# Kernel tuning notes

Hardware: AMD Instinct MI355X
Metric: run time of the kernel (lower is better)

The kernel has to match this reference:

```python
import jax, jax.numpy as jnp
import numpy as np

NUM_CLASSES = 10
CLS_W, L1_W, GIOU_W = 2.0, 5.0, 2.0


def box_cxcywh_to_xyxy(b):
    cx, cy, w, h = b[..., 0], b[..., 1], b[..., 2], b[..., 3]
    return jnp.stack([cx - w / 2, cy - h / 2, cx + w / 2, cy + h / 2], axis=-1)


def giou_matrix(b1, b2):
    # b1: (B,N,4), b2: (B,M,4) xyxy -> (B,N,M)
    a1 = jnp.clip(b1[..., 2] - b1[..., 0], 0) * jnp.clip(b1[..., 3] - b1[..., 1], 0)
    a2 = jnp.clip(b2[..., 2] - b2[..., 0], 0) * jnp.clip(b2[..., 3] - b2[..., 1], 0)
    lt = jnp.maximum(b1[..., :, None, :2], b2[..., None, :, :2])
    rb = jnp.minimum(b1[..., :, None, 2:], b2[..., None, :, 2:])
    wh = jnp.clip(rb - lt, 0)
    inter = wh[..., 0] * wh[..., 1]
    union = a1[..., :, None] + a2[..., None, :] - inter
    iou = inter / jnp.clip(union, 1e-6)
    lte = jnp.minimum(b1[..., :, None, :2], b2[..., None, :, :2])
    rbe = jnp.maximum(b1[..., :, None, 2:], b2[..., None, :, 2:])
    whe = jnp.clip(rbe - lte, 0)
    enc = whe[..., 0] * whe[..., 1]
    return iou - (enc - union) / jnp.clip(enc, 1e-6)


def giou_elem(b1, b2):
    # b1, b2: (N,4) xyxy, paired -> (N,)
    a1 = jnp.clip(b1[:, 2] - b1[:, 0], 0) * jnp.clip(b1[:, 3] - b1[:, 1], 0)
    a2 = jnp.clip(b2[:, 2] - b2[:, 0], 0) * jnp.clip(b2[:, 3] - b2[:, 1], 0)
    lt = jnp.maximum(b1[:, :2], b2[:, :2])
    rb = jnp.minimum(b1[:, 2:], b2[:, 2:])
    wh = jnp.clip(rb - lt, 0)
    inter = wh[:, 0] * wh[:, 1]
    union = a1 + a2 - inter
    iou = inter / jnp.clip(union, 1e-6)
    lte = jnp.minimum(b1[:, :2], b2[:, :2])
    rbe = jnp.maximum(b1[:, 2:], b2[:, 2:])
    whe = jnp.clip(rbe - lte, 0)
    enc = whe[:, 0] * whe[:, 1]
    return iou - (enc - union) / jnp.clip(enc, 1e-6)


def hungarian(cost):
    # Jonker-Volgenant style shortest-augmenting-path assignment (== scipy.linear_sum_assignment)
    cost = np.asarray(cost, dtype=np.float64)
    transposed = cost.shape[0] > cost.shape[1]
    C = cost.T if transposed else cost
    n, m = C.shape  # n <= m
    u = np.zeros(n + 1)
    v = np.zeros(m + 1)
    p = np.zeros(m + 1, dtype=np.int64)
    colr = np.arange(m + 1)
    for i in range(1, n + 1):
        p[0] = i
        j0 = 0
        minv = np.full(m + 1, np.inf)
        way = np.zeros(m + 1, dtype=np.int64)
        used = np.zeros(m + 1, dtype=bool)
        while True:
            used[j0] = True
            i0 = p[j0]
            unused = colr[1:][~used[1:]]
            cur = C[i0 - 1, unused - 1] - u[i0] - v[unused]
            better = cur < minv[unused]
            bidx = unused[better]
            minv[bidx] = cur[better]
            way[bidx] = j0
            j1 = unused[np.argmin(minv[unused])]
            delta = minv[j1]
            u[p[used]] += delta
            v[used] -= delta
            minv[~used] -= delta
            j0 = j1
            if p[j0] == 0:
                break
        while j0 != 0:
            jn = way[j0]
            p[j0] = p[jn]
            j0 = jn
    rows = p[1:] - 1
    cols = np.arange(m)
    sel = rows >= 0
    r, c = rows[sel], cols[sel]
    if transposed:
        r, c = c, r
    order = np.argsort(r)
    return r[order], c[order]


def compute_matches(pred_logits, pred_boxes, gt_classes, gt_boxes):
    # Batched cost matrices on device, per-sample Hungarian on host (mirrors torch.no_grad matcher).
    B, Q, _ = pred_logits.shape
    G = gt_classes.shape[1]
    prob = jax.nn.softmax(pred_logits, axis=-1)
    cls_idx = jnp.clip(gt_classes, 0, NUM_CLASSES - 1)
    idx = jnp.broadcast_to(cls_idx[:, None, :], (B, Q, G))
    cls_cost = -jnp.take_along_axis(prob, idx, axis=2)                 # (B,Q,G)
    l1_cost = jnp.abs(pred_boxes[:, :, None, :] - gt_boxes[:, None, :, :]).sum(-1)
    g = giou_matrix(box_cxcywh_to_xyxy(pred_boxes), box_cxcywh_to_xyxy(gt_boxes))
    cost = CLS_W * cls_cost + L1_W * l1_cost - GIOU_W * g
    cost_np = np.asarray(jax.device_get(cost))
    valid_np = np.asarray(jax.device_get(gt_classes)) >= 0
    bs, ps, gs = [], [], []
    for bi in range(B):
        vidx = np.nonzero(valid_np[bi])[0]
        if vidx.size == 0:
            continue
        r, c = hungarian(cost_np[bi][:, vidx])
        bs.append(np.full(r.size, bi, dtype=np.int64))
        ps.append(r.astype(np.int64))
        gs.append(vidx[c].astype(np.int64))
    if bs:
        return np.concatenate(bs), np.concatenate(ps), np.concatenate(gs)
    z = np.zeros(0, np.int64)
    return z, z, z


def detection_loss(pred_logits, pred_boxes, gt_boxes, target_cls, b_f, p_f, g_f, n_matched):
    C1 = pred_logits.shape[-1]
    logp = jax.nn.log_softmax(pred_logits, axis=-1).reshape(-1, C1)
    t = target_cls.reshape(-1)
    w = jnp.ones(C1, dtype=pred_logits.dtype).at[-1].set(0.1)
    nll = -jnp.take_along_axis(logp, t[:, None], axis=1)[:, 0]
    wt = w[t]
    cls_loss = (wt * nll).sum() / wt.sum()
    mp = pred_boxes[b_f, p_f]
    mg = gt_boxes[b_f, g_f]
    l1 = jnp.abs(mp - mg).sum()
    gd = giou_elem(box_cxcywh_to_xyxy(mp), box_cxcywh_to_xyxy(mg))
    gl = (1.0 - gd).sum()
    return CLS_W * cls_loss + L1_W * l1 / n_matched + GIOU_W * gl / n_matched


def setup_inputs() -> dict:
    key = jax.random.key(0)
    k1, k2, k3, k4, k5 = jax.random.split(key, 5)
    B, Q, G, C = 64, 900, 100, NUM_CLASSES
    pred_logits = jax.random.normal(k1, (B, Q, C + 1), dtype=jnp.float32)
    pred_boxes = jax.random.uniform(k2, (B, Q, 4), dtype=jnp.float32, minval=0.05, maxval=0.6)
    gt_boxes = jax.random.uniform(k3, (B, G, 4), dtype=jnp.float32, minval=0.05, maxval=0.6)
    cls = jax.random.randint(k4, (B, G), 0, C)
    nvalid = jax.random.randint(k5, (B,), 1, G + 1)
    mask = jnp.arange(G)[None, :] < nvalid[:, None]
    gt_classes = jnp.where(mask, cls, -1).astype(jnp.int32)
    return {"pred_logits": pred_logits, "pred_boxes": pred_boxes,
            "gt_classes": gt_classes, "gt_boxes": gt_boxes}


def reference(pred_logits, pred_boxes, gt_classes, gt_boxes):
    B, Q = pred_logits.shape[:2]
    b_f, p_f, g_f = compute_matches(pred_logits, pred_boxes, gt_classes, gt_boxes)
    gt_np = np.asarray(jax.device_get(gt_classes))
    tc = np.full((B, Q), NUM_CLASSES, dtype=np.int32)
    tc[b_f, p_f] = gt_np[b_f, g_f]
    n_matched = max(int(b_f.size), 1)
    return detection_loss(pred_logits, pred_boxes, gt_boxes, jnp.asarray(tc), b_f, p_f, g_f, n_matched)
```

## Files before the change

### kernel.cpp

```cpp
#include <hip/hip_runtime.h>
#include <hip/hip_bf16.h>
#include <math.h>

#define BB 64
#define QQ 900
#define GG 100
#define NCLS 10
#define CP1 11

#define STRIDE 960
#define KPL 15
#define NT 512
#define NW 8
#define QMASK 255
#define ROUND_CAP 20000

#define NCH 8
#define QCH 128

#define CLS_W 2.0f
#define L1_W 5.0f
#define GIOU_W 2.0f

struct Accum {
  double wnll, wt, l1, gl;
  int nm, counter;
  int pad[6];
};

__global__ __launch_bounds__(256) void cost_kernel(
    const float* __restrict__ logits, const float* __restrict__ pboxes,
    const int* __restrict__ gcls, const float* __restrict__ gboxes,
    float* __restrict__ cost, float4* __restrict__ part, Accum* acc) {
  const int b = blockIdx.y;
  const int chunk = blockIdx.x;
  const int tid = threadIdx.x;
  const int ql = tid & (QCH - 1);
  const int gh = tid >> 7;
  const int q = chunk * QCH + ql;

  if (chunk == 0 && b == 0 && tid == 0) {
    acc->wnll = 0.0; acc->wt = 0.0; acc->l1 = 0.0; acc->gl = 0.0;
    acc->nm = 0; acc->counter = 0;
  }

  __shared__ float s_gb[GG * 4];
  __shared__ int   s_gc[GG];
  __shared__ float s_prob[QCH * 13];
  __shared__ float s_c[GG][QCH + 1];
  __shared__ int   sh_n;

  if (tid == 0) sh_n = 0;
  __syncthreads();

  for (int i = tid; i < GG * 4; i += 256) s_gb[i] = gboxes[b * GG * 4 + i];
  for (int i = tid; i < GG; i += 256) {
    const int v = gcls[b * GG + i];
    s_gc[i] = v;
    if (v >= 0) atomicAdd(&sh_n, 1);
  }

  float pcx = 0.f, pcy = 0.f, pw = 0.f, ph = 0.f;
  if (q < QQ) {
    const float* pb = pboxes + ((size_t)b * QQ + q) * 4;
    pcx = pb[0]; pcy = pb[1]; pw = pb[2]; ph = pb[3];
    if (gh == 0) {
      const float* lg = logits + ((size_t)b * QQ + q) * CP1;
      float l[CP1];
      float mx = -1e30f;
      for (int c = 0; c < CP1; ++c) { l[c] = lg[c]; mx = fmaxf(mx, l[c]); }
      float se = 0.f;
      for (int c = 0; c < CP1; ++c) { l[c] = expf(l[c] - mx); se += l[c]; }
      const float inv = 1.0f / se;
      for (int c = 0; c < NCLS; ++c) s_prob[ql * 13 + c] = l[c] * inv;
    }
  }
  __syncthreads();
  const int sn = sh_n;

  const float px1 = pcx - 0.5f * pw, py1 = pcy - 0.5f * ph;
  const float px2 = pcx + 0.5f * pw, py2 = pcy + 0.5f * ph;
  const float pa = fmaxf(px2 - px1, 0.f) * fmaxf(py2 - py1, 0.f);

  float* crow = cost + ((size_t)b * GG) * STRIDE + q;
  for (int g = gh; g < sn; g += 2) {
    float cv = 3e38f;
    if (q < QQ) {
      int cls = s_gc[g];
      cls = cls < 0 ? 0 : (cls > NCLS - 1 ? NCLS - 1 : cls);
      const float cc = -s_prob[ql * 13 + cls];
      const float gcx = s_gb[g * 4 + 0], gcy = s_gb[g * 4 + 1];
      const float gw  = s_gb[g * 4 + 2], gh2 = s_gb[g * 4 + 3];
      const float l1 = fabsf(pcx - gcx) + fabsf(pcy - gcy) + fabsf(pw - gw) + fabsf(ph - gh2);
      const float gx1 = gcx - 0.5f * gw, gy1 = gcy - 0.5f * gh2;
      const float gx2 = gcx + 0.5f * gw, gy2 = gcy + 0.5f * gh2;
      const float ga = fmaxf(gx2 - gx1, 0.f) * fmaxf(gy2 - gy1, 0.f);
      const float ltx = fmaxf(px1, gx1), lty = fmaxf(py1, gy1);
      const float rbx = fminf(px2, gx2), rby = fminf(py2, gy2);
      const float iw = fmaxf(rbx - ltx, 0.f), ih = fmaxf(rby - lty, 0.f);
      const float inter = iw * ih;
      const float uni = pa + ga - inter;
      const float iou = inter / fmaxf(uni, 1e-6f);
      const float ex1 = fminf(px1, gx1), ey1 = fminf(py1, gy1);
      const float ex2 = fmaxf(px2, gx2), ey2 = fmaxf(py2, gy2);
      const float ew = fmaxf(ex2 - ex1, 0.f), eh = fmaxf(ey2 - ey1, 0.f);
      const float enc = ew * eh;
      const float giou = iou - (enc - uni) / fmaxf(enc, 1e-6f);
      cv = CLS_W * cc + L1_W * l1 - GIOU_W * giou;
      crow[(size_t)g * STRIDE] = cv;
    } else if (q < STRIDE) {
      crow[(size_t)g * STRIDE] = 1e30f;
    }
    s_c[g][ql] = cv;
  }
  __syncthreads();

  if (tid < sn) {
    const int kmax = (chunk == NCH - 1) ? (QQ - (NCH - 1) * QCH) : QCH;
    float m1 = 3e38f, m2 = 3e38f, n1 = 3e38f, n2 = 3e38f;
    int j1 = 0x7FFFFFFF, i1 = 0x7FFFFFFF;
    const int ka = kmax < 64 ? kmax : 64;
    for (int k = 0; k < ka; ++k) {
      const float c = s_c[tid][k];
      if (c < m1) { m2 = m1; m1 = c; j1 = 1 + chunk * QCH + k; }
      else if (c < m2) m2 = c;
    }
    for (int k = 64; k < kmax; ++k) {
      const float c = s_c[tid][k];
      if (c < n1) { n2 = n1; n1 = c; i1 = 1 + chunk * QCH + k; }
      else if (c < n2) n2 = c;
    }
    if (n1 < m1) { m2 = fminf(m1, n2); m1 = n1; j1 = i1; }
    else m2 = fminf(m2, n1);
    part[((size_t)b * NCH + chunk) * QCH + tid] = make_float4(m1, m2, __int_as_float(j1), 0.f);
  }
}

__global__ __launch_bounds__(NT) void jv_kernel(
    const float* __restrict__ logits, const float* __restrict__ pboxes,
    const int* __restrict__ gcls, const float* __restrict__ gboxes,
    const float* __restrict__ cost, const float4* __restrict__ part,
    Accum* acc, float* out) {
  const int b = blockIdx.x;
  const int tid = threadIdx.x;
  const int lane = tid & 63;
  const int w = tid >> 6;

  __shared__ float vl[STRIDE + 2];
  __shared__ int   p[QQ + 1];
  __shared__ unsigned long long way64[STRIDE + 2];
  __shared__ float m1l[GG + 1], m2l[GG + 1];
  __shared__ int   aminl[GG + 1];
  __shared__ int   s_gc[GG];
  __shared__ int   queue[QMASK + 1];
  __shared__ int   sh_n, sh_qtail, sh_head;
  __shared__ double r0[NW], r1[NW], r2[NW], r3[NW];
  __shared__ int r4[NW];
  __shared__ float s_lse[QQ], s_mx[QQ];

  if (tid == 0) { sh_n = 0; sh_qtail = 0; sh_head = 0; }
  for (int j = tid; j <= QQ; j += NT) p[j] = 0;
  for (int j = tid; j < STRIDE + 2; j += NT) { vl[j] = 0.f; way64[j] = 0ull; }
  if (tid < GG) s_gc[tid] = gcls[b * GG + tid];
  __syncthreads();
  if (tid < GG && s_gc[tid] >= 0) atomicAdd(&sh_n, 1);
  __syncthreads();
  const int n = sh_n;
  const float* Cb = cost + (size_t)b * GG * STRIDE;

  for (int r = tid; r < n; r += NT) {
    float m1 = 3e38f, m2 = 3e38f;
    int j1 = 0x7FFFFFFF;
#pragma unroll
    for (int ch = 0; ch < NCH; ++ch) {
      const float4 pr = part[((size_t)b * NCH + ch) * QCH + r];
      const float pm1 = pr.x, pm2 = pr.y;
      if (pm1 < m1) { m2 = fminf(m1, pm2); m1 = pm1; j1 = __float_as_int(pr.z); }
      else m2 = fminf(m2, pm1);
    }
    m1l[r] = m1; m2l[r] = m2; aminl[r] = j1;
  }
  for (int qq = tid; qq < QQ; qq += NT) {
    const float* lg = logits + ((size_t)b * QQ + qq) * CP1;
    float l[CP1];
    float mx = -1e30f;
    for (int c = 0; c < CP1; ++c) { l[c] = lg[c]; mx = fmaxf(mx, l[c]); }
    float se = 0.f;
    for (int c = 0; c < CP1; ++c) se += expf(l[c] - mx);
    s_mx[qq] = mx;
    s_lse[qq] = logf(se);
  }
  __syncthreads();

  if (tid < n) {
    const float regret = m2l[tid] - m1l[tid];
    const unsigned long long key =
        ((unsigned long long)__float_as_uint(regret) << 20) | (unsigned long long)(tid + 1);
    atomicMax(&way64[aminl[tid]], key);
  }
  __syncthreads();
  if (tid < n) {
    const int j1 = aminl[tid];
    if ((int)(way64[j1] & 0xFFFFFu) == tid + 1) {
      p[j1] = tid + 1;
      vl[j1] = m1l[tid] - m2l[tid];
    } else {
      const int t0 = atomicAdd(&sh_qtail, 1);
      queue[t0 & QMASK] = tid + 1;
    }
  }
  __syncthreads();

  {
    float pf[KPL];
    int pf_ok = 0, pf_rid = 0;
    int rounds = 0;
    while (rounds < ROUND_CAP) {
      const int head = sh_head, tail = sh_qtail;
      const int nq = tail - head;
      if (nq <= 0) break;
      const int take = nq < NW ? nq : NW;
      float m1 = 3e38f, m2 = 3e38f;
      int j1 = 0x7FFFFFFF, rid = 0;
      if (w < take) {
        float rc[KPL];
        if (pf_ok) {
          rid = pf_rid;
#pragma unroll
          for (int k = 0; k < KPL; ++k) rc[k] = pf[k];
        } else {
          rid = queue[(head + w) & QMASK];
          const float* Cr = Cb + (size_t)(rid - 1) * STRIDE + lane;
#pragma unroll
          for (int k = 0; k < KPL; ++k) rc[k] = Cr[k << 6];
        }
        float n1 = 3e38f, n2 = 3e38f;
        int i1 = 0x7FFFFFFF;
#pragma unroll
        for (int k = 0; k < 8; ++k) {
          const float c = rc[k] - vl[1 + lane + (k << 6)];
          if (c < m1) { m2 = m1; m1 = c; j1 = 1 + lane + (k << 6); }
          else if (c < m2) m2 = c;
        }
#pragma unroll
        for (int k = 8; k < KPL; ++k) {
          const float c = rc[k] - vl[1 + lane + (k << 6)];
          if (c < n1) { n2 = n1; n1 = c; i1 = 1 + lane + (k << 6); }
          else if (c < n2) n2 = c;
        }
        if (n1 < m1) { m2 = fminf(m1, n2); m1 = n1; j1 = i1; }
        else m2 = fminf(m2, n1);
        for (int m = 1; m < 64; m <<= 1) {
          const float o1 = __shfl_xor(m1, m);
          const float o2 = __shfl_xor(m2, m);
          const int oj = __shfl_xor(j1, m);
          if (o1 < m1) { m2 = fminf(m1, o2); m1 = o1; j1 = oj; }
          else m2 = fminf(m2, o1);
        }
      }
      pf_ok = 0;
      const int npos = head + take + w;
      if (npos < tail) {
        pf_rid = queue[npos & QMASK];
        const float* Cr = Cb + (size_t)(pf_rid - 1) * STRIDE + lane;
#pragma unroll
        for (int k = 0; k < KPL; ++k) pf[k] = Cr[k << 6];
        pf_ok = 1;
      }
      if (take > 1) {
        if (w < take && lane == 0) way64[j1] = 0ull;
        __syncthreads();
        if (w < take && lane == 0) {
          float d = m2 - m1;
          if (d < 0.f) d = 0.f;
          const unsigned long long key =
              ((unsigned long long)__float_as_uint(d) << 20) | (unsigned long long)rid;
          atomicMax(&way64[j1], key);
        }
        __syncthreads();
      }
      if (w < take && lane == 0) {
        if (take == 1 || (int)(way64[j1] & 0xFFFFFu) == rid) {
          float d = m2 - m1;
          if (d < 0.f) d = 0.f;
          const float ov = vl[j1];
          float nv = ov - d;
          if (!(nv < ov)) nv = nextafterf(ov, -3e38f);
          vl[j1] = nv;
          const int k0 = p[j1];
          p[j1] = rid;
          if (k0 > 0) { const int t0 = atomicAdd(&sh_qtail, 1); queue[t0 & QMASK] = k0; }
        } else {
          const int t0 = atomicAdd(&sh_qtail, 1);
          queue[t0 & QMASK] = rid;
        }
      }
      if (tid == 0) sh_head = head + take;
      ++rounds;
      __syncthreads();
    }
  }
  __syncthreads();

  double wnll = 0.0, wt = 0.0, l1d = 0.0, gld = 0.0;
  int nm = 0;
  for (int q = tid; q < QQ; q += NT) {
    const int idx = b * QQ + q;
    const int g = p[q + 1] - 1;
    const int t = (g >= 0) ? s_gc[g] : NCLS;
    const float lt = logits[(size_t)idx * CP1 + t];
    const float logp = (lt - s_mx[q]) - s_lse[q];
    const float wgt = (t == NCLS) ? 0.1f : 1.0f;
    wnll += (double)(wgt * (-logp));
    wt += (double)wgt;
    if (g >= 0) {
      nm += 1;
      const float* pb = pboxes + (size_t)idx * 4;
      const float* gb = gboxes + ((size_t)b * GG + g) * 4;
      const float pcx = pb[0], pcy = pb[1], pw = pb[2], ph = pb[3];
      const float gcx = gb[0], gcy = gb[1], gw = gb[2], gh = gb[3];
      const float l1 = fabsf(pcx - gcx) + fabsf(pcy - gcy) + fabsf(pw - gw) + fabsf(ph - gh);
      const float px1 = pcx - 0.5f * pw, py1 = pcy - 0.5f * ph;
      const float px2 = pcx + 0.5f * pw, py2 = pcy + 0.5f * ph;
      const float gx1 = gcx - 0.5f * gw, gy1 = gcy - 0.5f * gh;
      const float gx2 = gcx + 0.5f * gw, gy2 = gcy + 0.5f * gh;
      const float pa = fmaxf(px2 - px1, 0.f) * fmaxf(py2 - py1, 0.f);
      const float ga = fmaxf(gx2 - gx1, 0.f) * fmaxf(gy2 - gy1, 0.f);
      const float ltx = fmaxf(px1, gx1), lty = fmaxf(py1, gy1);
      const float rbx = fminf(px2, gx2), rby = fminf(py2, gy2);
      const float iw = fmaxf(rbx - ltx, 0.f), ih = fmaxf(rby - lty, 0.f);
      const float inter = iw * ih;
      const float uni = pa + ga - inter;
      const float iou = inter / fmaxf(uni, 1e-6f);
      const float ex1 = fminf(px1, gx1), ey1 = fminf(py1, gy1);
      const float ex2 = fmaxf(px2, gx2), ey2 = fmaxf(py2, gy2);
      const float ew = fmaxf(ex2 - ex1, 0.f), eh = fmaxf(ey2 - ey1, 0.f);
      const float enc = ew * eh;
      const float giou = iou - (enc - uni) / fmaxf(enc, 1e-6f);
      l1d += (double)l1;
      gld += (double)(1.0f - giou);
    }
  }

  for (int off = 32; off; off >>= 1) {
    wnll += __shfl_down(wnll, off);
    wt   += __shfl_down(wt, off);
    l1d  += __shfl_down(l1d, off);
    gld  += __shfl_down(gld, off);
    nm   += __shfl_down(nm, off);
  }
  if (lane == 0) { r0[w] = wnll; r1[w] = wt; r2[w] = l1d; r3[w] = gld; r4[w] = nm; }
  __syncthreads();
  if (tid == 0) {
    for (int x = 1; x < NW; ++x) { wnll += r0[x]; wt += r1[x]; l1d += r2[x]; gld += r3[x]; nm += r4[x]; }
    atomicAdd(&acc->wnll, wnll);
    atomicAdd(&acc->wt, wt);
    atomicAdd(&acc->l1, l1d);
    atomicAdd(&acc->gl, gld);
    atomicAdd(&acc->nm, nm);
    __threadfence();
    const int ticket = atomicAdd(&acc->counter, 1);
    if (ticket == BB - 1) {
      const double fw = atomicAdd(&acc->wnll, 0.0);
      const double fwt = atomicAdd(&acc->wt, 0.0);
      const double fl1 = atomicAdd(&acc->l1, 0.0);
      const double fgl = atomicAdd(&acc->gl, 0.0);
      int fnm = atomicAdd(&acc->nm, 0);
      if (fnm < 1) fnm = 1;
      const double loss = (double)CLS_W * (fw / fwt) +
                          ((double)L1_W * fl1 + (double)GIOU_W * fgl) / (double)fnm;
      out[0] = (float)loss;
    }
  }
}

extern "C" void kernel_launch(void* const* d_in, const int* in_sizes, int n_in,
                              void* d_out, int out_size, void* d_ws, size_t ws_size,
                              hipStream_t stream) {
  const float* logits = (const float*)d_in[0];
  const float* pboxes = (const float*)d_in[1];
  const int*   gcls   = (const int*)d_in[2];
  const float* gboxes = (const float*)d_in[3];

  char* ws = (char*)d_ws;
  Accum* acc = (Accum*)ws;
  float4* part = (float4*)(ws + 4096);
  float* cost = (float*)(ws + 4096 + (size_t)BB * NCH * QCH * sizeof(float4));

  cost_kernel<<<dim3(NCH, BB), 256, 0, stream>>>(logits, pboxes, gcls, gboxes, cost, part, acc);
  jv_kernel<<<BB, NT, 0, stream>>>(logits, pboxes, gcls, gboxes, cost, part, acc, (float*)d_out);
}
```

Baseline: 105.0 us.

## Process two auction rows per wave and drop per-round way64 clearing syncs

The auction loop in the JV kernel now has each wave bid for two queued rows per round, so up to 16 rows are handled per round instead of 8. Round-tagged atomicMax keys (round number in the high bits) replace the per-round clear of way64 and its two extra barriers, leaving one barrier per round. The cost kernel's per-row top-2 scan is also split across two thread halves and merged through shared memory. In exchange it uses more registers for double prefetch buffers, shrinks the row-id field to 12 bits, and processing more rows in parallel may cause more bid conflicts and re-queues.

```diff
diff --git a/kernel.cpp b/kernel.cpp
--- a/kernel.cpp
+++ b/kernel.cpp
@@ -48,6 +48,8 @@
   __shared__ int   s_gc[GG];
   __shared__ float s_prob[QCH * 13];
   __shared__ float s_c[GG][QCH + 1];
+  __shared__ float pm1[2][GG], pm2[2][GG];
+  __shared__ int   pj1[2][GG];
   __shared__ int   sh_n;
 
   if (tid == 0) sh_n = 0;
@@ -115,24 +117,32 @@
   }
   __syncthreads();
 
-  if (tid < sn) {
+  {
     const int kmax = (chunk == NCH - 1) ? (QQ - (NCH - 1) * QCH) : QCH;
-    float m1 = 3e38f, m2 = 3e38f, n1 = 3e38f, n2 = 3e38f;
-    int j1 = 0x7FFFFFFF, i1 = 0x7FFFFFFF;
-    const int ka = kmax < 64 ? kmax : 64;
-    for (int k = 0; k < ka; ++k) {
-      const float c = s_c[tid][k];
-      if (c < m1) { m2 = m1; m1 = c; j1 = 1 + chunk * QCH + k; }
-      else if (c < m2) m2 = c;
-    }
-    for (int k = 64; k < kmax; ++k) {
-      const float c = s_c[tid][k];
-      if (c < n1) { n2 = n1; n1 = c; i1 = 1 + chunk * QCH + k; }
-      else if (c < n2) n2 = c;
-    }
-    if (n1 < m1) { m2 = fminf(m1, n2); m1 = n1; j1 = i1; }
-    else m2 = fminf(m2, n1);
-    part[((size_t)b * NCH + chunk) * QCH + tid] = make_float4(m1, m2, __int_as_float(j1), 0.f);
+    const int half = tid >> 7;
+    const int r = tid & 127;
+    if (r < sn) {
+      const int k0 = half ? 64 : 0;
+      const int k1 = half ? kmax : (kmax < 64 ? kmax : 64);
+      float m1 = 3e38f, m2 = 3e38f;
+      int j1 = 0x7FFFFFFF;
+      for (int k = k0; k < k1; ++k) {
+        const float c = s_c[r][k];
+        if (c < m1) { m2 = m1; m1 = c; j1 = 1 + chunk * QCH + k; }
+        else if (c < m2) m2 = c;
+      }
+      pm1[half][r] = m1; pm2[half][r] = m2; pj1[half][r] = j1;
+    }
+    __syncthreads();
+    if (tid < sn) {
+      float m1 = pm1[0][tid], m2 = pm2[0][tid];
+      int j1 = pj1[0][tid];
+      const float n1 = pm1[1][tid], n2 = pm2[1][tid];
+      const int i1 = pj1[1][tid];
+      if (n1 < m1) { m2 = fminf(m1, n2); m1 = n1; j1 = i1; }
+      else m2 = fminf(m2, n1);
+      part[((size_t)b * NCH + chunk) * QCH + tid] = make_float4(m1, m2, __int_as_float(j1), 0.f);
+    }
   }
 }
 
@@ -210,93 +220,153 @@
     }
   }
   __syncthreads();
+  for (int j = tid; j < STRIDE + 2; j += NT) way64[j] = 0ull;
+  __syncthreads();
 
   {
-    float pf[KPL];
-    int pf_ok = 0, pf_rid = 0;
-    int rounds = 0;
-    while (rounds < ROUND_CAP) {
+    float pfA[KPL], pfB[KPL];
+    int pfAok = 0, pfBok = 0, pfArid = 0, pfBrid = 0;
+    int kround = 0;
+    while (kround < ROUND_CAP) {
       const int head = sh_head, tail = sh_qtail;
       const int nq = tail - head;
       if (nq <= 0) break;
-      const int take = nq < NW ? nq : NW;
-      float m1 = 3e38f, m2 = 3e38f;
-      int j1 = 0x7FFFFFFF, rid = 0;
-      if (w < take) {
-        float rc[KPL];
-        if (pf_ok) {
-          rid = pf_rid;
-#pragma unroll
-          for (int k = 0; k < KPL; ++k) rc[k] = pf[k];
+      const int take = nq < 2 * NW ? nq : 2 * NW;
+      ++kround;
+      const bool doA = (2 * w < take);
+      const bool doB = (2 * w + 1 < take);
+      int ridA = 0, ridB = 0;
+      float m1A = 3e38f, m2A = 3e38f, m1B = 3e38f, m2B = 3e38f;
+      int j1A = 0x7FFFFFFF, j1B = 0x7FFFFFFF;
+      if (doA) {
+        float rcA[KPL], rcB[KPL];
+        if (pfAok) { ridA = pfArid;
+#pragma unroll
+          for (int k = 0; k < KPL; ++k) rcA[k] = pfA[k];
         } else {
-          rid = queue[(head + w) & QMASK];
-          const float* Cr = Cb + (size_t)(rid - 1) * STRIDE + lane;
-#pragma unroll
-          for (int k = 0; k < KPL; ++k) rc[k] = Cr[k << 6];
-        }
-        float n1 = 3e38f, n2 = 3e38f;
-        int i1 = 0x7FFFFFFF;
+          ridA = queue[(head + 2 * w) & QMASK];
+          const float* Cr = Cb + (size_t)(ridA - 1) * STRIDE + lane;
+#pragma unroll
+          for (int k = 0; k < KPL; ++k) rcA[k] = Cr[k << 6];
+        }
+        if (doB) {
+          if (pfBok) { ridB = pfBrid;
+#pragma unroll
+            for (int k = 0; k < KPL; ++k) rcB[k] = pfB[k];
+          } else {
+            ridB = queue[(head + 2 * w + 1) & QMASK];
+            const float* Cr = Cb + (size_t)(ridB - 1) * STRIDE + lane;
+#pragma unroll
+            for (int k = 0; k < KPL; ++k) rcB[k] = Cr[k << 6];
+          }
+        } else {
+#pragma unroll
+          for (int k = 0; k < KPL; ++k) rcB[k] = 3e38f;
+        }
+        float nA1 = 3e38f, nA2 = 3e38f, nB1 = 3e38f, nB2 = 3e38f;
+        int iA1 = 0x7FFFFFFF, iB1 = 0x7FFFFFFF;
 #pragma unroll
         for (int k = 0; k < 8; ++k) {
-          const float c = rc[k] - vl[1 + lane + (k << 6)];
-          if (c < m1) { m2 = m1; m1 = c; j1 = 1 + lane + (k << 6); }
-          else if (c < m2) m2 = c;
+          const float vv = vl[1 + lane + (k << 6)];
+          const float cA = rcA[k] - vv;
+          if (cA < m1A) { m2A = m1A; m1A = cA; j1A = 1 + lane + (k << 6); }
+          else if (cA < m2A) m2A = cA;
+          const float cB = rcB[k] - vv;
+          if (cB < m1B) { m2B = m1B; m1B = cB; j1B = 1 + lane + (k << 6); }
+          else if (cB < m2B) m2B = cB;
         }
 #pragma unroll
         for (int k = 8; k < KPL; ++k) {
-          const float c = rc[k] - vl[1 + lane + (k << 6)];
-          if (c < n1) { n2 = n1; n1 = c; i1 = 1 + lane + (k << 6); }
-          else if (c < n2) n2 = c;
-        }
-        if (n1 < m1) { m2 = fminf(m1, n2); m1 = n1; j1 = i1; }
-        else m2 = fminf(m2, n1);
+          const float vv = vl[1 + lane + (k << 6)];
+          const float cA = rcA[k] - vv;
+          if (cA < nA1) { nA2 = nA1; nA1 = cA; iA1 = 1 + lane + (k << 6); }
+          else if (cA < nA2) nA2 = cA;
+          const float cB = rcB[k] - vv;
+          if (cB < nB1) { nB2 = nB1; nB1 = cB; iB1 = 1 + lane + (k << 6); }
+          else if (cB < nB2) nB2 = cB;
+        }
+        if (nA1 < m1A) { m2A = fminf(m1A, nA2); m1A = nA1; j1A = iA1; }
+        else m2A = fminf(m2A, nA1);
+        if (nB1 < m1B) { m2B = fminf(m1B, nB2); m1B = nB1; j1B = iB1; }
+        else m2B = fminf(m2B, nB1);
         for (int m = 1; m < 64; m <<= 1) {
-          const float o1 = __shfl_xor(m1, m);
-          const float o2 = __shfl_xor(m2, m);
-          const int oj = __shfl_xor(j1, m);
-          if (o1 < m1) { m2 = fminf(m1, o2); m1 = o1; j1 = oj; }
-          else m2 = fminf(m2, o1);
+          const float oA1 = __shfl_xor(m1A, m), oA2 = __shfl_xor(m2A, m);
+          const int ojA = __shfl_xor(j1A, m);
+          const float oB1 = __shfl_xor(m1B, m), oB2 = __shfl_xor(m2B, m);
+          const int ojB = __shfl_xor(j1B, m);
+          if (oA1 < m1A) { m2A = fminf(m1A, oA2); m1A = oA1; j1A = ojA; }
+          else m2A = fminf(m2A, oA1);
+          if (oB1 < m1B) { m2B = fminf(m1B, oB2); m1B = oB1; j1B = ojB; }
+          else m2B = fminf(m2B, oB1);
+        }
+        if (lane == 0) {
+          float dA = m2A - m1A;
+          if (dA < 0.f) dA = 0.f;
+          const unsigned long long keyA = ((unsigned long long)kround << 44) |
+              ((unsigned long long)__float_as_uint(dA) << 12) | (unsigned long long)ridA;
+          atomicMax(&way64[j1A], keyA);
+          if (doB) {
+            float dB = m2B - m1B;
+            if (dB < 0.f) dB = 0.f;
+            const unsigned long long keyB = ((unsigned long long)kround << 44) |
+                ((unsigned long long)__float_as_uint(dB) << 12) | (unsigned long long)ridB;
+            atomicMax(&way64[j1B], keyB);
+          }
         }
       }
-      pf_ok = 0;
-      const int npos = head + take + w;
-      if (npos < tail) {
-        pf_rid = queue[npos & QMASK];
-        const float* Cr = Cb + (size_t)(pf_rid - 1) * STRIDE + lane;
-#pragma unroll
-        for (int k = 0; k < KPL; ++k) pf[k] = Cr[k << 6];
-        pf_ok = 1;
+      pfAok = 0; pfBok = 0;
+      {
+        const int nh = head + take;
+        const int pA = nh + 2 * w, pB = pA + 1;
+        if (pA < tail) {
+          pfArid = queue[pA & QMASK];
+          const float* Cr = Cb + (size_t)(pfArid - 1) * STRIDE + lane;
+#pragma unroll
+          for (int k = 0; k < KPL; ++k) pfA[k] = Cr[k << 6];
+          pfAok = 1;
+        }
+        if (pB < tail) {
+          pfBrid = queue[pB & QMASK];
+          const float* Cr = Cb + (size_t)(pfBrid - 1) * STRIDE + lane;
+#pragma unroll
+          for (int k = 0; k < KPL; ++k) pfB[k] = Cr[k << 6];
+          pfBok = 1;
+        }
       }
-      if (take > 1) {
-        if (w < take && lane == 0) way64[j1] = 0ull;
-        __syncthreads();
-        if (w < take && lane == 0) {
-          float d = m2 - m1;
-          if (d < 0.f) d = 0.f;
-          const unsigned long long key =
-              ((unsigned long long)__float_as_uint(d) << 20) | (unsigned long long)rid;
-          atomicMax(&way64[j1], key);
-        }
-        __syncthreads();
-      }
-      if (w < take && lane == 0) {
-        if (take == 1 || (int)(way64[j1] & 0xFFFFFu) == rid) {
-          float d = m2 - m1;
-          if (d < 0.f) d = 0.f;
-          const float ov = vl[j1];
-          float nv = ov - d;
+      __syncthreads();
+      if (lane == 0 && doA) {
+        if ((int)(way64[j1A] & 0xFFFu) == ridA) {
+          float dA = m2A - m1A;
+          if (dA < 0.f) dA = 0.f;
+          const float ov = vl[j1A];
+          float nv = ov - dA;
           if (!(nv < ov)) nv = nextafterf(ov, -3e38f);
-          vl[j1] = nv;
-          const int k0 = p[j1];
-          p[j1] = rid;
+          vl[j1A] = nv;
+          const int k0 = p[j1A];
+          p[j1A] = ridA;
           if (k0 > 0) { const int t0 = atomicAdd(&sh_qtail, 1); queue[t0 & QMASK] = k0; }
         } else {
           const int t0 = atomicAdd(&sh_qtail, 1);
-          queue[t0 & QMASK] = rid;
+          queue[t0 & QMASK] = ridA;
+        }
+        if (doB) {
+          if ((int)(way64[j1B] & 0xFFFu) == ridB) {
+            float dB = m2B - m1B;
+            if (dB < 0.f) dB = 0.f;
+            const float ov = vl[j1B];
+            float nv = ov - dB;
+            if (!(nv < ov)) nv = nextafterf(ov, -3e38f);
+            vl[j1B] = nv;
+            const int k0 = p[j1B];
+            p[j1B] = ridB;
+            if (k0 > 0) { const int t0 = atomicAdd(&sh_qtail, 1); queue[t0 & QMASK] = k0; }
+          } else {
+            const int t0 = atomicAdd(&sh_qtail, 1);
+            queue[t0 & QMASK] = ridB;
+          }
         }
       }
       if (tid == 0) sh_head = head + take;
-      ++rounds;
       __syncthreads();
     }
   }
```

Result: no change. 104.3 us (-0.7%).

## Fuse cost computation into assignment kernel and recompute costs on the fly

Applied to the files above, without the earlier changes.

Removes the separate cost kernel and the global cost matrix. Per-query softmax probabilities and box geometry are now staged in shared memory, and each cost cell is recomputed inside the auction/JV rounds instead of being read from global memory. The round conflict check now always uses an atomic key tagged with the round number, which removes the per-round reset and an extra barrier. This saves one kernel launch and the global memory traffic for the cost matrix, but adds recomputation arithmetic to every round and uses much more shared memory, which may lower occupancy.

```diff
diff --git a/kernel.cpp b/kernel.cpp
--- a/kernel.cpp
+++ b/kernel.cpp
@@ -1,5 +1,4 @@
 #include <hip/hip_runtime.h>
-#include <hip/hip_bf16.h>
 #include <math.h>
 
 #define BB 64
@@ -15,9 +14,6 @@
 #define QMASK 255
 #define ROUND_CAP 20000
 
-#define NCH 8
-#define QCH 128
-
 #define CLS_W 2.0f
 #define L1_W 5.0f
 #define GIOU_W 2.0f
@@ -28,167 +24,118 @@
   int pad[6];
 };
 
-__global__ __launch_bounds__(256) void cost_kernel(
-    const float* __restrict__ logits, const float* __restrict__ pboxes,
-    const int* __restrict__ gcls, const float* __restrict__ gboxes,
-    float* __restrict__ cost, float4* __restrict__ part, Accum* acc) {
-  const int b = blockIdx.y;
-  const int chunk = blockIdx.x;
-  const int tid = threadIdx.x;
-  const int ql = tid & (QCH - 1);
-  const int gh = tid >> 7;
-  const int q = chunk * QCH + ql;
-
-  if (chunk == 0 && b == 0 && tid == 0) {
-    acc->wnll = 0.0; acc->wt = 0.0; acc->l1 = 0.0; acc->gl = 0.0;
-    acc->nm = 0; acc->counter = 0;
-  }
-
-  __shared__ float s_gb[GG * 4];
-  __shared__ int   s_gc[GG];
-  __shared__ float s_prob[QCH * 13];
-  __shared__ float s_c[GG][QCH + 1];
-  __shared__ int   sh_n;
-
-  if (tid == 0) sh_n = 0;
-  __syncthreads();
-
-  for (int i = tid; i < GG * 4; i += 256) s_gb[i] = gboxes[b * GG * 4 + i];
-  for (int i = tid; i < GG; i += 256) {
-    const int v = gcls[b * GG + i];
-    s_gc[i] = v;
-    if (v >= 0) atomicAdd(&sh_n, 1);
-  }
-
-  float pcx = 0.f, pcy = 0.f, pw = 0.f, ph = 0.f;
-  if (q < QQ) {
-    const float* pb = pboxes + ((size_t)b * QQ + q) * 4;
-    pcx = pb[0]; pcy = pb[1]; pw = pb[2]; ph = pb[3];
-    if (gh == 0) {
-      const float* lg = logits + ((size_t)b * QQ + q) * CP1;
-      float l[CP1];
-      float mx = -1e30f;
-      for (int c = 0; c < CP1; ++c) { l[c] = lg[c]; mx = fmaxf(mx, l[c]); }
-      float se = 0.f;
-      for (int c = 0; c < CP1; ++c) { l[c] = expf(l[c] - mx); se += l[c]; }
-      const float inv = 1.0f / se;
-      for (int c = 0; c < NCLS; ++c) s_prob[ql * 13 + c] = l[c] * inv;
-    }
-  }
-  __syncthreads();
-  const int sn = sh_n;
-
-  const float px1 = pcx - 0.5f * pw, py1 = pcy - 0.5f * ph;
-  const float px2 = pcx + 0.5f * pw, py2 = pcy + 0.5f * ph;
-  const float pa = fmaxf(px2 - px1, 0.f) * fmaxf(py2 - py1, 0.f);
-
-  float* crow = cost + ((size_t)b * GG) * STRIDE + q;
-  for (int g = gh; g < sn; g += 2) {
-    float cv = 3e38f;
-    if (q < QQ) {
-      int cls = s_gc[g];
-      cls = cls < 0 ? 0 : (cls > NCLS - 1 ? NCLS - 1 : cls);
-      const float cc = -s_prob[ql * 13 + cls];
-      const float gcx = s_gb[g * 4 + 0], gcy = s_gb[g * 4 + 1];
-      const float gw  = s_gb[g * 4 + 2], gh2 = s_gb[g * 4 + 3];
-      const float l1 = fabsf(pcx - gcx) + fabsf(pcy - gcy) + fabsf(pw - gw) + fabsf(ph - gh2);
-      const float gx1 = gcx - 0.5f * gw, gy1 = gcy - 0.5f * gh2;
-      const float gx2 = gcx + 0.5f * gw, gy2 = gcy + 0.5f * gh2;
-      const float ga = fmaxf(gx2 - gx1, 0.f) * fmaxf(gy2 - gy1, 0.f);
-      const float ltx = fmaxf(px1, gx1), lty = fmaxf(py1, gy1);
-      const float rbx = fminf(px2, gx2), rby = fminf(py2, gy2);
-      const float iw = fmaxf(rbx - ltx, 0.f), ih = fmaxf(rby - lty, 0.f);
-      const float inter = iw * ih;
-      const float uni = pa + ga - inter;
-      const float iou = inter / fmaxf(uni, 1e-6f);
-      const float ex1 = fminf(px1, gx1), ey1 = fminf(py1, gy1);
-      const float ex2 = fmaxf(px2, gx2), ey2 = fmaxf(py2, gy2);
-      const float ew = fmaxf(ex2 - ex1, 0.f), eh = fmaxf(ey2 - ey1, 0.f);
-      const float enc = ew * eh;
-      const float giou = iou - (enc - uni) / fmaxf(enc, 1e-6f);
-      cv = CLS_W * cc + L1_W * l1 - GIOU_W * giou;
-      crow[(size_t)g * STRIDE] = cv;
-    } else if (q < STRIDE) {
-      crow[(size_t)g * STRIDE] = 1e30f;
-    }
-    s_c[g][ql] = cv;
-  }
-  __syncthreads();
-
-  if (tid < sn) {
-    const int kmax = (chunk == NCH - 1) ? (QQ - (NCH - 1) * QCH) : QCH;
-    float m1 = 3e38f, m2 = 3e38f, n1 = 3e38f, n2 = 3e38f;
-    int j1 = 0x7FFFFFFF, i1 = 0x7FFFFFFF;
-    const int ka = kmax < 64 ? kmax : 64;
-    for (int k = 0; k < ka; ++k) {
-      const float c = s_c[tid][k];
-      if (c < m1) { m2 = m1; m1 = c; j1 = 1 + chunk * QCH + k; }
-      else if (c < m2) m2 = c;
-    }
-    for (int k = 64; k < kmax; ++k) {
-      const float c = s_c[tid][k];
-      if (c < n1) { n2 = n1; n1 = c; i1 = 1 + chunk * QCH + k; }
-      else if (c < n2) n2 = c;
-    }
-    if (n1 < m1) { m2 = fminf(m1, n2); m1 = n1; j1 = i1; }
-    else m2 = fminf(m2, n1);
-    part[((size_t)b * NCH + chunk) * QCH + tid] = make_float4(m1, m2, __int_as_float(j1), 0.f);
-  }
-}
-
 __global__ __launch_bounds__(NT) void jv_kernel(
     const float* __restrict__ logits, const float* __restrict__ pboxes,
     const int* __restrict__ gcls, const float* __restrict__ gboxes,
-    const float* __restrict__ cost, const float4* __restrict__ part,
     Accum* acc, float* out) {
   const int b = blockIdx.x;
   const int tid = threadIdx.x;
   const int lane = tid & 63;
   const int w = tid >> 6;
 
-  __shared__ float vl[STRIDE + 2];
-  __shared__ int   p[QQ + 1];
+  __shared__ float  s_prob[QQ * NCLS];
+  __shared__ float4 s_pb4[QQ];
+  __shared__ float4 s_pxy[QQ];
+  __shared__ float  s_pa[QQ];
+  __shared__ float  s_gb[GG * 4];
+  __shared__ int    s_gc[GG];
+  __shared__ float  s_mx[QQ], s_lse[QQ];
+  __shared__ float  vl[STRIDE + 2];
+  __shared__ int    p[QQ + 1];
   __shared__ unsigned long long way64[STRIDE + 2];
-  __shared__ float m1l[GG + 1], m2l[GG + 1];
-  __shared__ int   aminl[GG + 1];
-  __shared__ int   s_gc[GG];
-  __shared__ int   queue[QMASK + 1];
-  __shared__ int   sh_n, sh_qtail, sh_head;
+  __shared__ float  m1l[GG], m2l[GG];
+  __shared__ int    aminl[GG];
+  __shared__ int    queue[QMASK + 1];
+  __shared__ int    sh_n, sh_qtail, sh_head;
   __shared__ double r0[NW], r1[NW], r2[NW], r3[NW];
-  __shared__ int r4[NW];
-  __shared__ float s_lse[QQ], s_mx[QQ];
+  __shared__ int    r4[NW];
 
   if (tid == 0) { sh_n = 0; sh_qtail = 0; sh_head = 0; }
   for (int j = tid; j <= QQ; j += NT) p[j] = 0;
   for (int j = tid; j < STRIDE + 2; j += NT) { vl[j] = 0.f; way64[j] = 0ull; }
+  for (int i = tid; i < GG * 4; i += NT) s_gb[i] = gboxes[b * GG * 4 + i];
   if (tid < GG) s_gc[tid] = gcls[b * GG + tid];
-  __syncthreads();
-  if (tid < GG && s_gc[tid] >= 0) atomicAdd(&sh_n, 1);
-  __syncthreads();
-  const int n = sh_n;
-  const float* Cb = cost + (size_t)b * GG * STRIDE;
-
-  for (int r = tid; r < n; r += NT) {
-    float m1 = 3e38f, m2 = 3e38f;
-    int j1 = 0x7FFFFFFF;
-#pragma unroll
-    for (int ch = 0; ch < NCH; ++ch) {
-      const float4 pr = part[((size_t)b * NCH + ch) * QCH + r];
-      const float pm1 = pr.x, pm2 = pr.y;
-      if (pm1 < m1) { m2 = fminf(m1, pm2); m1 = pm1; j1 = __float_as_int(pr.z); }
-      else m2 = fminf(m2, pm1);
-    }
-    m1l[r] = m1; m2l[r] = m2; aminl[r] = j1;
-  }
   for (int qq = tid; qq < QQ; qq += NT) {
+    const float4 pb = reinterpret_cast<const float4*>(pboxes)[(size_t)b * QQ + qq];
+    s_pb4[qq] = pb;
+    const float px1 = pb.x - 0.5f * pb.z, py1 = pb.y - 0.5f * pb.w;
+    const float px2 = pb.x + 0.5f * pb.z, py2 = pb.y + 0.5f * pb.w;
+    s_pxy[qq] = make_float4(px1, py1, px2, py2);
+    s_pa[qq] = fmaxf(px2 - px1, 0.f) * fmaxf(py2 - py1, 0.f);
     const float* lg = logits + ((size_t)b * QQ + qq) * CP1;
     float l[CP1];
     float mx = -1e30f;
     for (int c = 0; c < CP1; ++c) { l[c] = lg[c]; mx = fmaxf(mx, l[c]); }
     float se = 0.f;
-    for (int c = 0; c < CP1; ++c) se += expf(l[c] - mx);
+    for (int c = 0; c < CP1; ++c) { l[c] = expf(l[c] - mx); se += l[c]; }
+    const float inv = 1.0f / se;
+    for (int c = 0; c < NCLS; ++c) s_prob[qq * NCLS + c] = l[c] * inv;
     s_mx[qq] = mx;
     s_lse[qq] = logf(se);
+  }
+  __syncthreads();
+  if (tid < GG && s_gc[tid] >= 0) atomicAdd(&sh_n, 1);
+  __syncthreads();
+  const int n = sh_n;
+
+  auto cell = [&](int qv, int cls, float gcx, float gcy, float gwv, float ghv,
+                  float gx1, float gy1, float gx2, float gy2, float ga) -> float {
+    const float cc = -s_prob[qv * NCLS + cls];
+    const float4 pb = s_pb4[qv];
+    const float4 pxy = s_pxy[qv];
+    const float pa = s_pa[qv];
+    const float l1v = fabsf(pb.x - gcx) + fabsf(pb.y - gcy) +
+                      fabsf(pb.z - gwv) + fabsf(pb.w - ghv);
+    const float ltx = fmaxf(pxy.x, gx1), lty = fmaxf(pxy.y, gy1);
+    const float rbx = fminf(pxy.z, gx2), rby = fminf(pxy.w, gy2);
+    const float iw = fmaxf(rbx - ltx, 0.f), ih = fmaxf(rby - lty, 0.f);
+    const float inter = iw * ih;
+    const float uni = pa + ga - inter;
+    const float iou = inter / fmaxf(uni, 1e-6f);
+    const float ex1 = fminf(pxy.x, gx1), ey1 = fminf(pxy.y, gy1);
+    const float ex2 = fmaxf(pxy.z, gx2), ey2 = fmaxf(pxy.w, gy2);
+    const float ew = fmaxf(ex2 - ex1, 0.f), eh = fmaxf(ey2 - ey1, 0.f);
+    const float enc = ew * eh;
+    const float giou = iou - (enc - uni) / fmaxf(enc, 1e-6f);
+    return CLS_W * cc + L1_W * l1v - GIOU_W * giou;
+  };
+
+  for (int r = w; r < n; r += NW) {
+    int cls = s_gc[r];
+    cls = cls < 0 ? 0 : (cls > NCLS - 1 ? NCLS - 1 : cls);
+    const float gcx = s_gb[r * 4 + 0], gcy = s_gb[r * 4 + 1];
+    const float gwv = s_gb[r * 4 + 2], ghv = s_gb[r * 4 + 3];
+    const float gx1 = gcx - 0.5f * gwv, gy1 = gcy - 0.5f * ghv;
+    const float gx2 = gcx + 0.5f * gwv, gy2 = gcy + 0.5f * ghv;
+    const float ga = fmaxf(gx2 - gx1, 0.f) * fmaxf(gy2 - gy1, 0.f);
+    float m1 = 3e38f, m2 = 3e38f, n1 = 3e38f, n2 = 3e38f;
+    int j1 = 0x7FFFFFFF, i1 = 0x7FFFFFFF;
+#pragma unroll
+    for (int k = 0; k < 8; ++k) {
+      const int q = lane + (k << 6);
+      const float c = (q < QQ) ? cell(q, cls, gcx, gcy, gwv, ghv, gx1, gy1, gx2, gy2, ga)
+                               : 3e38f;
+      if (c < m1) { m2 = m1; m1 = c; j1 = 1 + q; }
+      else if (c < m2) m2 = c;
+    }
+#pragma unroll
+    for (int k = 8; k < KPL; ++k) {
+      const int q = lane + (k << 6);
+      const float c = (q < QQ) ? cell(q, cls, gcx, gcy, gwv, ghv, gx1, gy1, gx2, gy2, ga)
+                               : 3e38f;
+      if (c < n1) { n2 = n1; n1 = c; i1 = 1 + q; }
+      else if (c < n2) n2 = c;
+    }
+    if (n1 < m1) { m2 = fminf(m1, n2); m1 = n1; j1 = i1; }
+    else m2 = fminf(m2, n1);
+    for (int m = 1; m < 64; m <<= 1) {
+      const float o1 = __shfl_xor(m1, m);
+      const float o2 = __shfl_xor(m2, m);
+      const int oj = __shfl_xor(j1, m);
+      if (o1 < m1) { m2 = fminf(m1, o2); m1 = o1; j1 = oj; }
+      else m2 = fminf(m2, o1);
+    }
+    if (lane == 0) { m1l[r] = m1; m2l[r] = m2; aminl[r] = j1; }
   }
   __syncthreads();
 
@@ -210,42 +157,49 @@
     }
   }
   __syncthreads();
+  for (int j = tid; j < STRIDE + 2; j += NT) way64[j] = 0ull;
+  __syncthreads();
 
   {
-    float pf[KPL];
-    int pf_ok = 0, pf_rid = 0;
-    int rounds = 0;
-    while (rounds < ROUND_CAP) {
+    int kround = 0;
+    while (kround < ROUND_CAP) {
       const int head = sh_head, tail = sh_qtail;
       const int nq = tail - head;
       if (nq <= 0) break;
       const int take = nq < NW ? nq : NW;
+      ++kround;
+      const bool doA = (w < take);
+      int rid = 0;
       float m1 = 3e38f, m2 = 3e38f;
-      int j1 = 0x7FFFFFFF, rid = 0;
-      if (w < take) {
-        float rc[KPL];
-        if (pf_ok) {
-          rid = pf_rid;
-#pragma unroll
-          for (int k = 0; k < KPL; ++k) rc[k] = pf[k];
-        } else {
-          rid = queue[(head + w) & QMASK];
-          const float* Cr = Cb + (size_t)(rid - 1) * STRIDE + lane;
-#pragma unroll
-          for (int k = 0; k < KPL; ++k) rc[k] = Cr[k << 6];
-        }
+      int j1 = 0x7FFFFFFF;
+      if (doA) {
+        rid = queue[(head + w) & QMASK];
+        const int g = rid - 1;
+        int cls = s_gc[g];
+        cls = cls < 0 ? 0 : (cls > NCLS - 1 ? NCLS - 1 : cls);
+        const float gcx = s_gb[g * 4 + 0], gcy = s_gb[g * 4 + 1];
+        const float gwv = s_gb[g * 4 + 2], ghv = s_gb[g * 4 + 3];
+        const float gx1 = gcx - 0.5f * gwv, gy1 = gcy - 0.5f * ghv;
+        const float gx2 = gcx + 0.5f * gwv, gy2 = gcy + 0.5f * ghv;
+        const float ga = fmaxf(gx2 - gx1, 0.f) * fmaxf(gy2 - gy1, 0.f);
         float n1 = 3e38f, n2 = 3e38f;
         int i1 = 0x7FFFFFFF;
 #pragma unroll
         for (int k = 0; k < 8; ++k) {
-          const float c = rc[k] - vl[1 + lane + (k << 6)];
-          if (c < m1) { m2 = m1; m1 = c; j1 = 1 + lane + (k << 6); }
+          const int q = lane + (k << 6);
+          const float base = (q < QQ) ? cell(q, cls, gcx, gcy, gwv, ghv, gx1, gy1, gx2, gy2, ga)
+                                      : 1e30f;
+          const float c = base - vl[1 + q];
+          if (c < m1) { m2 = m1; m1 = c; j1 = 1 + q; }
           else if (c < m2) m2 = c;
         }
 #pragma unroll
         for (int k = 8; k < KPL; ++k) {
-          const float c = rc[k] - vl[1 + lane + (k << 6)];
-          if (c < n1) { n2 = n1; n1 = c; i1 = 1 + lane + (k << 6); }
+          const int q = lane + (k << 6);
+          const float base = (q < QQ) ? cell(q, cls, gcx, gcy, gwv, ghv, gx1, gy1, gx2, gy2, ga)
+                                      : 1e30f;
+          const float c = base - vl[1 + q];
+          if (c < n1) { n2 = n1; n1 = c; i1 = 1 + q; }
           else if (c < n2) n2 = c;
         }
         if (n1 < m1) { m2 = fminf(m1, n2); m1 = n1; j1 = i1; }
@@ -257,30 +211,17 @@
           if (o1 < m1) { m2 = fminf(m1, o2); m1 = o1; j1 = oj; }
           else m2 = fminf(m2, o1);
         }
-      }
-      pf_ok = 0;
-      const int npos = head + take + w;
-      if (npos < tail) {
-        pf_rid = queue[npos & QMASK];
-        const float* Cr = Cb + (size_t)(pf_rid - 1) * STRIDE + lane;
-#pragma unroll
-        for (int k = 0; k < KPL; ++k) pf[k] = Cr[k << 6];
-        pf_ok = 1;
-      }
-      if (take > 1) {
-        if (w < take && lane == 0) way64[j1] = 0ull;
-        __syncthreads();
-        if (w < take && lane == 0) {
+        if (lane == 0) {
           float d = m2 - m1;
           if (d < 0.f) d = 0.f;
-          const unsigned long long key =
-              ((unsigned long long)__float_as_uint(d) << 20) | (unsigned long long)rid;
+          const unsigned long long key = ((unsigned long long)kround << 44) |
+              ((unsigned long long)__float_as_uint(d) << 12) | (unsigned long long)rid;
           atomicMax(&way64[j1], key);
         }
-        __syncthreads();
       }
-      if (w < take && lane == 0) {
-        if (take == 1 || (int)(way64[j1] & 0xFFFFFu) == rid) {
+      __syncthreads();
+      if (lane == 0 && doA) {
+        if ((int)(way64[j1] & 0xFFFu) == rid) {
           float d = m2 - m1;
           if (d < 0.f) d = 0.f;
           const float ov = vl[j1];
@@ -296,7 +237,6 @@
         }
       }
       if (tid == 0) sh_head = head + take;
-      ++rounds;
       __syncthreads();
     }
   }
@@ -315,10 +255,10 @@
     wt += (double)wgt;
     if (g >= 0) {
       nm += 1;
-      const float* pb = pboxes + (size_t)idx * 4;
-      const float* gb = gboxes + ((size_t)b * GG + g) * 4;
-      const float pcx = pb[0], pcy = pb[1], pw = pb[2], ph = pb[3];
-      const float gcx = gb[0], gcy = gb[1], gw = gb[2], gh = gb[3];
+      const float4 pb = s_pb4[q];
+      const float pcx = pb.x, pcy = pb.y, pw = pb.z, ph = pb.w;
+      const float gcx = s_gb[g * 4 + 0], gcy = s_gb[g * 4 + 1];
+      const float gw = s_gb[g * 4 + 2], gh = s_gb[g * 4 + 3];
       const float l1 = fabsf(pcx - gcx) + fabsf(pcy - gcy) + fabsf(pw - gw) + fabsf(ph - gh);
       const float px1 = pcx - 0.5f * pw, py1 = pcy - 0.5f * ph;
       const float px2 = pcx + 0.5f * pw, py2 = pcy + 0.5f * ph;
@@ -384,9 +324,7 @@
 
   char* ws = (char*)d_ws;
   Accum* acc = (Accum*)ws;
-  float4* part = (float4*)(ws + 4096);
-  float* cost = (float*)(ws + 4096 + (size_t)BB * NCH * QCH * sizeof(float4));
-
-  cost_kernel<<<dim3(NCH, BB), 256, 0, stream>>>(logits, pboxes, gcls, gboxes, cost, part, acc);
-  jv_kernel<<<BB, NT, 0, stream>>>(logits, pboxes, gcls, gboxes, cost, part, acc, (float*)d_out);
+
+  hipMemsetAsync(acc, 0, 256, stream);
+  jv_kernel<<<BB, NT, 0, stream>>>(logits, pboxes, gcls, gboxes, acc, (float*)d_out);
 }
```

New measurement: 125.3 us. 1.19x slower.
